# Kernel tuning notes

Hardware: AMD Instinct MI355X
Metric: run time of the kernel (lower is better)

Reference implementation:

```python
import jax, jax.numpy as jnp
import numpy as np

B = 4096          # graphs in batch
NODES = 256       # nodes per graph
N = B * NODES     # total nodes
D = 64            # latent_dim
H = 128           # hidden
NEG = jnp.float32(np.finfo(np.float32).min)


def setup_inputs() -> dict:
    key = jax.random.key(0)
    ks = jax.random.split(key, 5)
    embed = jax.random.normal(ks[0], (N, D), jnp.float32)
    graph_embed = jax.random.normal(ks[1], (B, D), jnp.float32)
    prefix_sum = (jnp.arange(B, dtype=jnp.int32) + 1) * NODES  # cumulative node counts
    banned = jax.random.randint(ks[2], (N,), 0, 2) == 1        # per-node banned-action mask
    W1 = jax.random.normal(ks[3], (2 * D, H), jnp.float32) * 0.05
    b1 = jnp.zeros((H,), jnp.float32)
    W2 = jax.random.normal(ks[4], (H, 1), jnp.float32) * 0.05
    b2 = jnp.zeros((1,), jnp.float32)
    return dict(embed=embed, graph_embed=graph_embed, prefix_sum=prefix_sum,
                banned=banned, W1=W1, b1=b1, W2=W2, b2=b2)


def reference(embed, graph_embed, prefix_sum, banned, W1, b1, W2, b2):
    n = embed.shape[0]
    b = prefix_sum.shape[0]
    # node -> graph id (replaces rep_idx python loop in rep_global_embed)
    seg_ids = jnp.searchsorted(prefix_sum, jnp.arange(n, dtype=prefix_sum.dtype), side='right')
    g_rep = graph_embed[seg_ids]                                 # [N, D] gathered graph embed
    # linear_1 -> relu -> linear_out
    h = jax.nn.relu(jnp.concatenate([embed, g_rep], axis=1) @ W1 + b1)  # [N, H]
    raw_pred = h @ W2 + b2                                       # [N, 1]
    # greedy_actions: index_fill banned with float32 min, then per-graph argmax (jmax)
    q = jnp.where(banned, NEG, raw_pred[:, 0])                   # [N]
    seg_max = jax.ops.segment_max(q, seg_ids, num_segments=b)    # [B]
    is_max = q == seg_max[seg_ids]
    cand = jnp.where(is_max, jnp.arange(n), n)
    gidx = jax.ops.segment_min(cand, seg_ids, num_segments=b)    # global argmax per graph
    starts = jnp.concatenate([jnp.zeros((1,), prefix_sum.dtype), prefix_sum[:-1]])
    actions = gidx.astype(prefix_sum.dtype) - starts             # local (per-graph) action ids
    values = q[gidx]
    return actions, values, raw_pred
```

## Files before the change

kernel.cpp:

```cpp
#include <hip/hip_runtime.h>

#define NEGF (-3.402823466e+38f)
constexpr int BG = 4096;

typedef __attribute__((ext_vector_type(8))) short short8;
typedef __attribute__((ext_vector_type(4))) float f32x4;

constexpr int WT_STRIDE = 72;
constexpr int WT_ELEMS  = 128 * WT_STRIDE;

__device__ __forceinline__ void split_bf16(float a, short& hi, short& lo) {
    const unsigned u = __float_as_uint(a);
    hi = (short)(u >> 16);
    const float lof = a - __uint_as_float(u & 0xffff0000u);
    lo = (short)(__float_as_uint(lof) >> 16);
}

__global__ __launch_bounds__(256, 3) void k_main(
    const float* __restrict__ embed, const float* __restrict__ ge,
    const float* __restrict__ W1, const float* __restrict__ b1,
    const float* __restrict__ W2, const float* __restrict__ b2,
    const int* __restrict__ banned, float* __restrict__ out) {

    __shared__ __align__(16) unsigned short sW[2 * WT_ELEMS];
    __shared__ float s_ge[64];
    __shared__ float s_gp[2][128];
    __shared__ float s_gt[128];
    __shared__ float s_raw[256];
    __shared__ float s_rv[4];
    __shared__ int   s_ri[4];

    const int t = threadIdx.x;
    const int lane = t & 63;
    const int w = t >> 6;
    const int quad = lane >> 4;
    const int l15 = lane & 15;
    const int g = blockIdx.x;

    const int bn = banned[(size_t)g * 256 + t];

    const float* ebase0 = embed + ((size_t)g * 256 + w * 32 + l15) * 64 + quad * 8;
    f32x4 araw[2][4];
#pragma unroll
    for (int mt = 0; mt < 2; ++mt) {
        const float* p = ebase0 + mt * 16 * 64;
        araw[mt][0] = *(const f32x4*)p;
        araw[mt][1] = *(const f32x4*)(p + 4);
        araw[mt][2] = *(const f32x4*)(p + 32);
        araw[mt][3] = *(const f32x4*)(p + 36);
    }

    {
        const int j = t & 127, h = t >> 7;
        const float* src = W1 + (h * 32) * 128 + j;
        unsigned short* dhi = sW + j * WT_STRIDE + h * 32;
        unsigned short* dlo = dhi + WT_ELEMS;
#pragma unroll
        for (int i = 0; i < 4; ++i) {
            short8 hv, lv;
#pragma unroll
            for (int kc = 0; kc < 8; ++kc) {
                short hi, lo;
                split_bf16(src[(i * 8 + kc) * 128], hi, lo);
                hv[kc] = hi;
                lv[kc] = lo;
            }
            *(short8*)(dhi + i * 8) = hv;
            *(short8*)(dlo + i * 8) = lv;
        }
    }
    if (t < 64) s_ge[t] = ge[g * 64 + t];
    __syncthreads();

    {
        const int j = t & 127, h = t >> 7;
        float s = 0.f;
        const float* wb = W1 + (64 + h * 32) * 128 + j;
#pragma unroll
        for (int k = 0; k < 32; ++k) s = fmaf(s_ge[h * 32 + k], wb[k * 128], s);
        s_gp[h][j] = s;
    }
    __syncthreads();
    if (t < 128) s_gt[t] = s_gp[0][t] + s_gp[1][t] + b1[t];
    __syncthreads();

    const float b2v = b2[0];

#pragma unroll
    for (int iter = 0; iter < 2; ++iter) {
        if (iter == 1) {
            const float* ebase = embed + ((size_t)g * 256 + 128 + w * 32 + l15) * 64 + quad * 8;
#pragma unroll
            for (int mt = 0; mt < 2; ++mt) {
                const float* p = ebase + mt * 16 * 64;
                araw[mt][0] = *(const f32x4*)p;
                araw[mt][1] = *(const f32x4*)(p + 4);
                araw[mt][2] = *(const f32x4*)(p + 32);
                araw[mt][3] = *(const f32x4*)(p + 36);
            }
        }

        short8 ahi[2][2], alo[2][2];
#pragma unroll
        for (int mt = 0; mt < 2; ++mt)
#pragma unroll
            for (int kc = 0; kc < 2; ++kc)
#pragma unroll
                for (int i = 0; i < 8; ++i) {
                    const float a = (i < 4) ? araw[mt][kc * 2][i] : araw[mt][kc * 2 + 1][i - 4];
                    short hi, lo;
                    split_bf16(a, hi, lo);
                    ahi[mt][kc][i] = hi;
                    alo[mt][kc][i] = lo;
                }

        f32x4 acc[2][8];
#pragma unroll
        for (int mt = 0; mt < 2; ++mt)
#pragma unroll
            for (int nt = 0; nt < 8; ++nt) acc[mt][nt] = f32x4{0.f, 0.f, 0.f, 0.f};

#pragma unroll
        for (int nt = 0; nt < 8; ++nt) {
            const unsigned short* rowp = sW + (nt * 16 + l15) * WT_STRIDE + quad * 8;
            const short8 bhi0 = *(const short8*)rowp;
            const short8 bhi1 = *(const short8*)(rowp + 32);
            const short8 blo0 = *(const short8*)(rowp + WT_ELEMS);
            const short8 blo1 = *(const short8*)(rowp + WT_ELEMS + 32);
#pragma unroll
            for (int mt = 0; mt < 2; ++mt) {
                f32x4 c = acc[mt][nt];
                c = __builtin_amdgcn_mfma_f32_16x16x32_bf16(ahi[mt][0], bhi0, c, 0, 0, 0);
                c = __builtin_amdgcn_mfma_f32_16x16x32_bf16(ahi[mt][1], bhi1, c, 0, 0, 0);
                c = __builtin_amdgcn_mfma_f32_16x16x32_bf16(alo[mt][0], bhi0, c, 0, 0, 0);
                c = __builtin_amdgcn_mfma_f32_16x16x32_bf16(alo[mt][1], bhi1, c, 0, 0, 0);
                c = __builtin_amdgcn_mfma_f32_16x16x32_bf16(ahi[mt][0], blo0, c, 0, 0, 0);
                c = __builtin_amdgcn_mfma_f32_16x16x32_bf16(ahi[mt][1], blo1, c, 0, 0, 0);
                acc[mt][nt] = c;
            }
        }

#pragma unroll
        for (int mt = 0; mt < 2; ++mt) {
            float pr[4] = {0.f, 0.f, 0.f, 0.f};
#pragma unroll
            for (int nt = 0; nt < 8; ++nt) {
                const float gt = s_gt[nt * 16 + l15];
                const float w2 = W2[nt * 16 + l15];
#pragma unroll
                for (int r = 0; r < 4; ++r)
                    pr[r] = fmaf(fmaxf(acc[mt][nt][r] + gt, 0.f), w2, pr[r]);
            }
#pragma unroll
            for (int m = 1; m <= 8; m <<= 1)
#pragma unroll
                for (int r = 0; r < 4; ++r)
                    pr[r] += __shfl_xor(pr[r], m, 64);
            if (l15 == 0) {
                float* dst = s_raw + iter * 128 + w * 32 + mt * 16 + quad * 4;
                dst[0] = pr[0]; dst[1] = pr[1]; dst[2] = pr[2]; dst[3] = pr[3];
            }
        }
    }
    __syncthreads();

    const float rp = s_raw[t] + b2v;
    out[2 * BG + (size_t)g * 256 + t] = rp;
    float q = bn ? NEGF : rp;
    int idx = t;
#pragma unroll
    for (int off = 32; off >= 1; off >>= 1) {
        const float qv = __shfl_down(q, off, 64);
        const int iv = __shfl_down(idx, off, 64);
        if (qv > q || (qv == q && iv < idx)) { q = qv; idx = iv; }
    }
    if (lane == 0) { s_rv[w] = q; s_ri[w] = idx; }
    __syncthreads();
    if (t == 0) {
#pragma unroll
        for (int i = 1; i < 4; ++i)
            if (s_rv[i] > q || (s_rv[i] == q && s_ri[i] < idx)) { q = s_rv[i]; idx = s_ri[i]; }
        out[g] = (float)idx;
        out[BG + g] = q;
    }
}

extern "C" void kernel_launch(void* const* d_in, const int* in_sizes, int n_in,
                              void* d_out, int out_size, void* d_ws, size_t ws_size,
                              hipStream_t stream) {
    const float* embed  = (const float*)d_in[0];
    const float* gembed = (const float*)d_in[1];
    const int* banned   = (const int*)d_in[3];
    const float* W1     = (const float*)d_in[4];
    const float* b1     = (const float*)d_in[5];
    const float* W2     = (const float*)d_in[6];
    const float* b2     = (const float*)d_in[7];
    float* out = (float*)d_out;

    (void)d_ws; (void)ws_size;

    k_main<<<BG, 256, 0, stream>>>(embed, gembed, W1, b1, W2, b2, banned, out);
}
```

Measured before the change: 376.0 us.

## Process four graphs per block with pipelined embed loads and split accumulators

Each block now handles four graphs, so the W1 bf16 hi/lo split into shared memory and the graph-projection setup are amortised over more work. The next half-graph of embeddings is loaded into registers while the current half is being multiplied. MFMA accumulation uses two independent chains per tile with the epilogue fused in, and launch bounds ask for higher occupancy. The trade-offs are fewer blocks, more register pressure, and per-graph syncs inside the loop.

```diff
diff --git a/kernel.cpp b/kernel.cpp
--- a/kernel.cpp
+++ b/kernel.cpp
@@ -1,7 +1,8 @@
 #include <hip/hip_runtime.h>
 
 #define NEGF (-3.402823466e+38f)
-constexpr int BG = 4096;
+constexpr int BG  = 4096;
+constexpr int GPB = 4;
 
 typedef __attribute__((ext_vector_type(8))) short short8;
 typedef __attribute__((ext_vector_type(4))) float f32x4;
@@ -16,39 +17,106 @@
     lo = (short)(__float_as_uint(lof) >> 16);
 }
 
-__global__ __launch_bounds__(256, 3) void k_main(
+__device__ __forceinline__ void load_A(const float* __restrict__ embed, size_t node_base,
+                                       int w, int l15, int quad, f32x4 (&buf)[2][4]) {
+    const float* p0 = embed + (node_base + (size_t)(w * 32 + l15)) * 64 + quad * 8;
+#pragma unroll
+    for (int mt = 0; mt < 2; ++mt) {
+        const float* p = p0 + mt * 16 * 64;
+        buf[mt][0] = *(const f32x4*)p;
+        buf[mt][1] = *(const f32x4*)(p + 4);
+        buf[mt][2] = *(const f32x4*)(p + 32);
+        buf[mt][3] = *(const f32x4*)(p + 36);
+    }
+}
+
+__device__ __forceinline__ void convert_A(const f32x4 (&araw)[2][4],
+                                          short8 (&ahi)[2][2], short8 (&alo)[2][2]) {
+#pragma unroll
+    for (int mt = 0; mt < 2; ++mt)
+#pragma unroll
+        for (int kc = 0; kc < 2; ++kc)
+#pragma unroll
+            for (int i = 0; i < 8; ++i) {
+                const float a = (i < 4) ? araw[mt][kc * 2][i] : araw[mt][kc * 2 + 1][i - 4];
+                short hi, lo;
+                split_bf16(a, hi, lo);
+                ahi[mt][kc][i] = hi;
+                alo[mt][kc][i] = lo;
+            }
+}
+
+__device__ __forceinline__ void mfma_epi(const unsigned short* __restrict__ sW,
+                                         const short8 (&ahi)[2][2], const short8 (&alo)[2][2],
+                                         const float (&gtv)[8], const float (&w2v)[8],
+                                         float* __restrict__ s_raw,
+                                         int half, int w, int l15, int quad) {
+    float pr[2][4] = {{0.f, 0.f, 0.f, 0.f}, {0.f, 0.f, 0.f, 0.f}};
+#pragma unroll
+    for (int nt = 0; nt < 8; ++nt) {
+        const unsigned short* rowp = sW + (nt * 16 + l15) * WT_STRIDE + quad * 8;
+        const short8 bhi0 = *(const short8*)rowp;
+        const short8 bhi1 = *(const short8*)(rowp + 32);
+        const short8 blo0 = *(const short8*)(rowp + WT_ELEMS);
+        const short8 blo1 = *(const short8*)(rowp + WT_ELEMS + 32);
+#pragma unroll
+        for (int mt = 0; mt < 2; ++mt) {
+            f32x4 ca = {0.f, 0.f, 0.f, 0.f};
+            f32x4 cb = {0.f, 0.f, 0.f, 0.f};
+            ca = __builtin_amdgcn_mfma_f32_16x16x32_bf16(ahi[mt][0], bhi0, ca, 0, 0, 0);
+            cb = __builtin_amdgcn_mfma_f32_16x16x32_bf16(alo[mt][0], bhi0, cb, 0, 0, 0);
+            ca = __builtin_amdgcn_mfma_f32_16x16x32_bf16(ahi[mt][1], bhi1, ca, 0, 0, 0);
+            cb = __builtin_amdgcn_mfma_f32_16x16x32_bf16(alo[mt][1], bhi1, cb, 0, 0, 0);
+            cb = __builtin_amdgcn_mfma_f32_16x16x32_bf16(ahi[mt][0], blo0, cb, 0, 0, 0);
+            cb = __builtin_amdgcn_mfma_f32_16x16x32_bf16(ahi[mt][1], blo1, cb, 0, 0, 0);
+#pragma unroll
+            for (int r = 0; r < 4; ++r)
+                pr[mt][r] = fmaf(fmaxf(ca[r] + cb[r] + gtv[nt], 0.f), w2v[nt], pr[mt][r]);
+        }
+    }
+#pragma unroll
+    for (int m = 1; m <= 8; m <<= 1)
+#pragma unroll
+        for (int mt = 0; mt < 2; ++mt)
+#pragma unroll
+            for (int r = 0; r < 4; ++r)
+                pr[mt][r] += __shfl_xor(pr[mt][r], m, 64);
+    if (l15 == 0) {
+#pragma unroll
+        for (int mt = 0; mt < 2; ++mt) {
+            float* dst = s_raw + half * 128 + w * 32 + mt * 16 + quad * 4;
+            dst[0] = pr[mt][0]; dst[1] = pr[mt][1]; dst[2] = pr[mt][2]; dst[3] = pr[mt][3];
+        }
+    }
+}
+
+__global__ __launch_bounds__(256, 4) void k_main(
     const float* __restrict__ embed, const float* __restrict__ ge,
     const float* __restrict__ W1, const float* __restrict__ b1,
     const float* __restrict__ W2, const float* __restrict__ b2,
     const int* __restrict__ banned, float* __restrict__ out) {
 
     __shared__ __align__(16) unsigned short sW[2 * WT_ELEMS];
-    __shared__ float s_ge[64];
-    __shared__ float s_gp[2][128];
-    __shared__ float s_gt[128];
-    __shared__ float s_raw[256];
-    __shared__ float s_rv[4];
-    __shared__ int   s_ri[4];
+    __shared__ float s_misc[776];
+    float* s_ge  = s_misc;
+    float* s_raw = s_misc;
+    float* s_gt  = s_misc + 256;
+    float* s_rv  = s_misc + 768;
+    int*   s_ri  = (int*)(s_misc + 772);
 
     const int t = threadIdx.x;
     const int lane = t & 63;
     const int w = t >> 6;
     const int quad = lane >> 4;
     const int l15 = lane & 15;
-    const int g = blockIdx.x;
-
-    const int bn = banned[(size_t)g * 256 + t];
-
-    const float* ebase0 = embed + ((size_t)g * 256 + w * 32 + l15) * 64 + quad * 8;
-    f32x4 araw[2][4];
-#pragma unroll
-    for (int mt = 0; mt < 2; ++mt) {
-        const float* p = ebase0 + mt * 16 * 64;
-        araw[mt][0] = *(const f32x4*)p;
-        araw[mt][1] = *(const f32x4*)(p + 4);
-        araw[mt][2] = *(const f32x4*)(p + 32);
-        araw[mt][3] = *(const f32x4*)(p + 36);
-    }
+    const int g0 = blockIdx.x * GPB;
+
+    f32x4 A0[2][4], A1[2][4];
+    load_A(embed, (size_t)g0 * 256, w, l15, quad, A0);
+
+    float w2v[8];
+#pragma unroll
+    for (int nt = 0; nt < 8; ++nt) w2v[nt] = W2[nt * 16 + l15];
 
     {
         const int j = t & 127, h = t >> 7;
@@ -69,119 +137,70 @@
             *(short8*)(dlo + i * 8) = lv;
         }
     }
-    if (t < 64) s_ge[t] = ge[g * 64 + t];
+    s_ge[t] = ge[g0 * 64 + t];
     __syncthreads();
 
     {
-        const int j = t & 127, h = t >> 7;
-        float s = 0.f;
-        const float* wb = W1 + (64 + h * 32) * 128 + j;
-#pragma unroll
-        for (int k = 0; k < 32; ++k) s = fmaf(s_ge[h * 32 + k], wb[k * 128], s);
-        s_gp[h][j] = s;
+        const int j = t & 127;
+        const int gp = (t >> 7) * 2;
+        float a0 = 0.f, a1 = 0.f;
+        const float* wb = W1 + 64 * 128 + j;
+#pragma unroll 8
+        for (int k = 0; k < 64; ++k) {
+            const float wv = wb[k * 128];
+            a0 = fmaf(s_ge[gp * 64 + k], wv, a0);
+            a1 = fmaf(s_ge[gp * 64 + 64 + k], wv, a1);
+        }
+        const float b1j = b1[j];
+        s_gt[gp * 128 + j] = a0 + b1j;
+        s_gt[(gp + 1) * 128 + j] = a1 + b1j;
     }
     __syncthreads();
-    if (t < 128) s_gt[t] = s_gp[0][t] + s_gp[1][t] + b1[t];
-    __syncthreads();
 
     const float b2v = b2[0];
 
-#pragma unroll
-    for (int iter = 0; iter < 2; ++iter) {
-        if (iter == 1) {
-            const float* ebase = embed + ((size_t)g * 256 + 128 + w * 32 + l15) * 64 + quad * 8;
-#pragma unroll
-            for (int mt = 0; mt < 2; ++mt) {
-                const float* p = ebase + mt * 16 * 64;
-                araw[mt][0] = *(const f32x4*)p;
-                araw[mt][1] = *(const f32x4*)(p + 4);
-                araw[mt][2] = *(const f32x4*)(p + 32);
-                araw[mt][3] = *(const f32x4*)(p + 36);
-            }
-        }
+    for (int gi = 0; gi < GPB; ++gi) {
+        const int g = g0 + gi;
+        const size_t gn = (size_t)g * 256;
+
+        const int bn = banned[gn + t];
+        load_A(embed, gn + 128, w, l15, quad, A1);
+
+        float gtv[8];
+#pragma unroll
+        for (int nt = 0; nt < 8; ++nt) gtv[nt] = s_gt[gi * 128 + nt * 16 + l15];
 
         short8 ahi[2][2], alo[2][2];
-#pragma unroll
-        for (int mt = 0; mt < 2; ++mt)
-#pragma unroll
-            for (int kc = 0; kc < 2; ++kc)
-#pragma unroll
-                for (int i = 0; i < 8; ++i) {
-                    const float a = (i < 4) ? araw[mt][kc * 2][i] : araw[mt][kc * 2 + 1][i - 4];
-                    short hi, lo;
-                    split_bf16(a, hi, lo);
-                    ahi[mt][kc][i] = hi;
-                    alo[mt][kc][i] = lo;
-                }
-
-        f32x4 acc[2][8];
-#pragma unroll
-        for (int mt = 0; mt < 2; ++mt)
-#pragma unroll
-            for (int nt = 0; nt < 8; ++nt) acc[mt][nt] = f32x4{0.f, 0.f, 0.f, 0.f};
-
-#pragma unroll
-        for (int nt = 0; nt < 8; ++nt) {
-            const unsigned short* rowp = sW + (nt * 16 + l15) * WT_STRIDE + quad * 8;
-            const short8 bhi0 = *(const short8*)rowp;
-            const short8 bhi1 = *(const short8*)(rowp + 32);
-            const short8 blo0 = *(const short8*)(rowp + WT_ELEMS);
-            const short8 blo1 = *(const short8*)(rowp + WT_ELEMS + 32);
-#pragma unroll
-            for (int mt = 0; mt < 2; ++mt) {
-                f32x4 c = acc[mt][nt];
-                c = __builtin_amdgcn_mfma_f32_16x16x32_bf16(ahi[mt][0], bhi0, c, 0, 0, 0);
-                c = __builtin_amdgcn_mfma_f32_16x16x32_bf16(ahi[mt][1], bhi1, c, 0, 0, 0);
-                c = __builtin_amdgcn_mfma_f32_16x16x32_bf16(alo[mt][0], bhi0, c, 0, 0, 0);
-                c = __builtin_amdgcn_mfma_f32_16x16x32_bf16(alo[mt][1], bhi1, c, 0, 0, 0);
-                c = __builtin_amdgcn_mfma_f32_16x16x32_bf16(ahi[mt][0], blo0, c, 0, 0, 0);
-                c = __builtin_amdgcn_mfma_f32_16x16x32_bf16(ahi[mt][1], blo1, c, 0, 0, 0);
-                acc[mt][nt] = c;
-            }
-        }
-
-#pragma unroll
-        for (int mt = 0; mt < 2; ++mt) {
-            float pr[4] = {0.f, 0.f, 0.f, 0.f};
-#pragma unroll
-            for (int nt = 0; nt < 8; ++nt) {
-                const float gt = s_gt[nt * 16 + l15];
-                const float w2 = W2[nt * 16 + l15];
-#pragma unroll
-                for (int r = 0; r < 4; ++r)
-                    pr[r] = fmaf(fmaxf(acc[mt][nt][r] + gt, 0.f), w2, pr[r]);
-            }
-#pragma unroll
-            for (int m = 1; m <= 8; m <<= 1)
-#pragma unroll
-                for (int r = 0; r < 4; ++r)
-                    pr[r] += __shfl_xor(pr[r], m, 64);
-            if (l15 == 0) {
-                float* dst = s_raw + iter * 128 + w * 32 + mt * 16 + quad * 4;
-                dst[0] = pr[0]; dst[1] = pr[1]; dst[2] = pr[2]; dst[3] = pr[3];
-            }
-        }
-    }
-    __syncthreads();
-
-    const float rp = s_raw[t] + b2v;
-    out[2 * BG + (size_t)g * 256 + t] = rp;
-    float q = bn ? NEGF : rp;
-    int idx = t;
-#pragma unroll
-    for (int off = 32; off >= 1; off >>= 1) {
-        const float qv = __shfl_down(q, off, 64);
-        const int iv = __shfl_down(idx, off, 64);
-        if (qv > q || (qv == q && iv < idx)) { q = qv; idx = iv; }
-    }
-    if (lane == 0) { s_rv[w] = q; s_ri[w] = idx; }
-    __syncthreads();
-    if (t == 0) {
-#pragma unroll
-        for (int i = 1; i < 4; ++i)
-            if (s_rv[i] > q || (s_rv[i] == q && s_ri[i] < idx)) { q = s_rv[i]; idx = s_ri[i]; }
-        out[g] = (float)idx;
-        out[BG + g] = q;
+
+        convert_A(A0, ahi, alo);
+        mfma_epi(sW, ahi, alo, gtv, w2v, s_raw, 0, w, l15, quad);
+
+        convert_A(A1, ahi, alo);
+        if (gi < GPB - 1)
+            load_A(embed, gn + 256, w, l15, quad, A0);
+        mfma_epi(sW, ahi, alo, gtv, w2v, s_raw, 1, w, l15, quad);
+
+        __syncthreads();
+
+        const float rp = s_raw[t] + b2v;
+        out[2 * BG + gn + t] = rp;
+        float q = bn ? NEGF : rp;
+        int idx = t;
+#pragma unroll
+        for (int off = 32; off >= 1; off >>= 1) {
+            const float qv = __shfl_down(q, off, 64);
+            const int iv = __shfl_down(idx, off, 64);
+            if (qv > q || (qv == q && iv < idx)) { q = qv; idx = iv; }
+        }
+        if (lane == 0) { s_rv[w] = q; s_ri[w] = idx; }
+        __syncthreads();
+        if (t == 0) {
+#pragma unroll
+            for (int i = 1; i < 4; ++i)
+                if (s_rv[i] > q || (s_rv[i] == q && s_ri[i] < idx)) { q = s_rv[i]; idx = s_ri[i]; }
+            out[g] = (float)idx;
+            out[BG + g] = q;
+        }
     }
 }
 
@@ -199,5 +218,5 @@
 
     (void)d_ws; (void)ws_size;
 
-    k_main<<<BG, 256, 0, stream>>>(embed, gembed, W1, b1, W2, b2, banned, out);
-}
+    k_main<<<BG / GPB, 256, 0, stream>>>(embed, gembed, W1, b1, W2, b2, banned, out);
+}
```

New measurement: 863.6 us. +129.7%, slower.
